# Optimization experiments

Measured on AMD Instinct MI355X. Metric: run time of the kernel, lower is better.

Reference implementation:

```python
import jax, jax.numpy as jnp
import numpy as np

LOG2PI = 1.8378770664093453
KL_WEIGHT = 1.0
N_OBS = 2_000_000
N_REFL = 250_000
N_IMG = 2000
MC = 32
N_OPS = 2
D_META = 6
D_EMB = 32
D_IN = 2 + 2 + D_META + 2 + D_EMB  # Imodel(2) + Iscale(2) + metadata(6) + wavelength + 1/d^2 + image embed
HIDDEN = 64


def weighted_pearson(x, y, w):
    z = 1.0 / w.sum(-1)
    mx = z * (w * x).sum(-1)
    my = z * (w * y).sum(-1)
    dx = x - mx
    dy = y - my
    cxy = z * (w * dx * dy).sum(-1)
    cx = z * (w * dx * dx).sum(-1)
    cy = z * (w * dy * dy).sum(-1)
    return cxy / jnp.sqrt(cx * cy)


def setup_inputs() -> dict:
    key = jax.random.key(0)
    ks = jax.random.split(key, 16)
    I = jax.random.normal(ks[0], (N_OBS, 1), jnp.float32)
    SigI = jax.random.uniform(ks[1], (N_OBS, 1), jnp.float32, 0.5, 1.5)
    image_id = jnp.sort(jax.random.randint(ks[2], (N_OBS,), 0, N_IMG, jnp.int32))
    metadata = jax.random.normal(ks[3], (N_OBS, D_META), jnp.float32)
    wavelength = 1.0 + 0.1 * jax.random.uniform(ks[4], (N_OBS, 1), jnp.float32)
    dHKL = jax.random.uniform(ks[5], (N_OBS, 1), jnp.float32, 1.0, 4.0)
    refl_ids = jax.random.randint(ks[6], (N_OPS, N_OBS), 0, N_REFL, jnp.int32)
    q_loc = jax.random.normal(ks[7], (N_REFL,), jnp.float32)
    q_scale_raw = 0.1 * jax.random.normal(ks[8], (N_REFL,), jnp.float32)
    img_emb = 0.1 * jax.random.normal(ks[9], (N_IMG, D_EMB), jnp.float32)
    W1 = jax.random.normal(ks[10], (D_IN, HIDDEN), jnp.float32) / np.sqrt(D_IN)
    b1 = jnp.zeros((HIDDEN,), jnp.float32)
    W2 = jax.random.normal(ks[11], (HIDDEN, 2), jnp.float32) / np.sqrt(HIDDEN)
    b2 = jnp.zeros((2,), jnp.float32)
    zeps = jax.random.normal(ks[12], (MC, N_REFL), jnp.float32)
    seps = jax.random.normal(ks[13], (N_OBS, MC), jnp.float32)
    return dict(I=I, SigI=SigI, image_id=image_id, metadata=metadata,
                wavelength=wavelength, dHKL=dHKL, refl_ids=refl_ids,
                q_loc=q_loc, q_scale_raw=q_scale_raw, img_emb=img_emb,
                W1=W1, b1=b1, W2=W2, b2=b2, zeps=zeps, seps=seps)


def reference(I, SigI, image_id, metadata, wavelength, dHKL, refl_ids,
              q_loc, q_scale_raw, img_emb, W1, b1, W2, b2, zeps, seps):
    n_images = img_emb.shape[0]
    sq = jax.nn.softplus(q_scale_raw)                         # q.stddev  [n_refl]
    # KL(N(q_loc, sq) || N(0, 1)), analytic, averaged over reflections
    kl_div = (-jnp.log(sq) + 0.5 * (sq * sq + q_loc * q_loc) - 0.5).mean()
    meta = jnp.concatenate([metadata, wavelength, 1.0 / jnp.square(dHKL)], -1)  # [N, 8]
    Iscale = jnp.concatenate([I, SigI], -1)                   # [N, 2]
    Imodel = jnp.stack([q_loc, sq], -1)                       # [n_refl, 2]
    zT = (q_loc[None, :] + sq[None, :] * zeps).T              # rsample, [n_refl, mc]
    emb = img_emb[image_id]                                   # [N, d_emb]
    ll_list, Ipred_list = [], []
    for op in range(refl_ids.shape[0]):                       # small fixed op count
        rid = refl_ids[op]                                    # [N]
        _Imodel = Imodel[rid]                                 # gather  [N, 2]
        feats = jnp.concatenate([_Imodel, Iscale, meta, emb], -1)
        h = jax.nn.relu(feats @ W1 + b1)
        loc_ls = h @ W2 + b2                                  # [N, 2]
        scale = loc_ls[:, :1] + jax.nn.softplus(loc_ls[:, 1:]) * seps  # [N, mc]
        _Ipred = zT[rid] * scale                              # gather * scale [N, mc]
        _ll = -0.5 * jnp.square((_Ipred - I) / SigI) - jnp.log(SigI) - 0.5 * LOG2PI
        _ll = jax.ops.segment_sum(_ll, image_id, num_segments=n_images)  # [n_img, mc]
        ll_list.append(_ll.mean(-1))                          # [n_img]
        Ipred_list.append(_Ipred.mean(-1))                    # [N]
    ll = jnp.stack(ll_list, -1)                               # [n_img, n_ops]
    ll_max = ll.max(-1)
    op_idx = ll.argmax(-1)                                    # [n_img]
    elbo = -ll_max.mean() + KL_WEIGHT * kl_div
    Ipred = jnp.stack(Ipred_list, -1)                         # [N, n_ops]
    sel = jnp.take_along_axis(Ipred, op_idx[image_id][:, None], -1)[:, 0]
    w = 1.0 / jnp.square(SigI)
    cc = weighted_pearson(I[:, 0], sel, w[:, 0])
    return jnp.stack([elbo, cc])
```

## Files before the change

kernel.cpp:

```cpp
#include <hip/hip_runtime.h>
#include <hip/hip_fp16.h>
#include <math.h>

#define N_OBS_C 2000000
#define N_REFL_C 250000
#define N_IMG_C 2000
#define MC_C 32
#define HID 64
#define NSLOT 16
#define LOG2PI_F 1.8378770664093453f


typedef float f2 __attribute__((ext_vector_type(2)));

__device__ __forceinline__ void pkfma(f2& d, f2 a, f2 b) {
    asm("v_pk_fma_f32 %0, %1, %2, %0" : "+v"(d) : "v"(a), "v"(b));
}
__device__ __forceinline__ f2 pkfma3(f2 a, f2 b, f2 c) {
    f2 d;
    asm("v_pk_fma_f32 %0, %1, %2, %3" : "=v"(d) : "v"(a), "v"(b), "v"(c));
    return d;
}

__device__ __forceinline__ float softplusf(float x) {
    return (x > 20.f) ? x : log1pf(expf(x));
}

#define ZERO_F4 96004
__global__ __launch_bounds__(256) void k_zero(float4* __restrict__ p) {
    int i = blockIdx.x * 256 + threadIdx.x;
    if (i < ZERO_F4) p[i] = make_float4(0.f, 0.f, 0.f, 0.f);
}

__global__ __launch_bounds__(256) void k_refl(const float* __restrict__ q_loc,
                                              const float* __restrict__ q_scale_raw,
                                              const float* __restrict__ zeps,
                                              float* __restrict__ sq,
                                              __half* __restrict__ zT,
                                              double* __restrict__ kl_sum) {
    int r = blockIdx.x * 256 + threadIdx.x;
    double kl = 0.0;
    if (r < N_REFL_C) {
        float ql = q_loc[r];
        float sp = softplusf(q_scale_raw[r]);
        sq[r] = sp;
        kl = (double)(-logf(sp) + 0.5f * (sp * sp + ql * ql) - 0.5f);
        float z[MC_C];
#pragma unroll
        for (int m = 0; m < MC_C; ++m)
            z[m] = fmaf(sp, zeps[(size_t)m * N_REFL_C + r], ql);
        uint4* outp = (uint4*)(zT + (size_t)r * MC_C);
#pragma unroll
        for (int q = 0; q < 4; ++q) {
            __half2 h0 = __floats2half2_rn(z[8 * q + 0], z[8 * q + 1]);
            __half2 h1 = __floats2half2_rn(z[8 * q + 2], z[8 * q + 3]);
            __half2 h2 = __floats2half2_rn(z[8 * q + 4], z[8 * q + 5]);
            __half2 h3 = __floats2half2_rn(z[8 * q + 6], z[8 * q + 7]);
            outp[q] = make_uint4(*(unsigned*)&h0, *(unsigned*)&h1,
                                 *(unsigned*)&h2, *(unsigned*)&h3);
        }
    }
    for (int o = 32; o > 0; o >>= 1) kl += __shfl_xor(kl, o);
    __shared__ double skl[4];
    int lane = threadIdx.x & 63, w = threadIdx.x >> 6;
    if (lane == 0) skl[w] = kl;
    __syncthreads();
    if (threadIdx.x == 0) atomicAdd(kl_sum, skl[0] + skl[1] + skl[2] + skl[3]);
}

__global__ __launch_bounds__(64) void k_imgpre(const float* __restrict__ img_emb,
                                               const float* __restrict__ W1,
                                               const float* __restrict__ b1,
                                               float* __restrict__ img_pre) {
    int g = blockIdx.x;
    int j = threadIdx.x;
    float acc = b1[j];
#pragma unroll
    for (int e = 0; e < 32; ++e)
        acc = fmaf(img_emb[g * 32 + e], W1[(12 + e) * HID + j], acc);
    img_pre[g * HID + j] = acc;
}

__global__ __launch_bounds__(256) void k_mlp(const float* __restrict__ I,
                                             const float* __restrict__ SigI,
                                             const int* __restrict__ image_id,
                                             const float* __restrict__ metadata,
                                             const float* __restrict__ wavelength,
                                             const float* __restrict__ dHKL,
                                             const int* __restrict__ refl_ids,
                                             const float* __restrict__ q_loc,
                                             const float* __restrict__ W1,
                                             const float* __restrict__ W2,
                                             const float* __restrict__ b2,
                                             const float* __restrict__ sq,
                                             const float* __restrict__ img_pre,
                                             float4* __restrict__ params) {
    __shared__ float sW1[12 * HID];
    __shared__ float sW2a[HID], sW2b[HID];
    for (int t = threadIdx.x; t < 12 * HID; t += 256) sW1[t] = W1[t];
    if (threadIdx.x < HID) {
        sW2a[threadIdx.x] = W2[threadIdx.x * 2 + 0];
        sW2b[threadIdx.x] = W2[threadIdx.x * 2 + 1];
    }
    __syncthreads();

    int n0 = blockIdx.x * 512 + threadIdx.x;
    int n1 = n0 + 256;
    bool a0 = (n0 < N_OBS_C), a1 = (n1 < N_OBS_C);
    int m0 = a0 ? n0 : (N_OBS_C - 1);
    int m1 = a1 ? n1 : (N_OBS_C - 1);

    f2 f0p[10], f1p[10];
    {
        float v;
        v = I[m0];            f0p[0].x = v; f0p[0].y = v;
        v = SigI[m0];         f0p[1].x = v; f0p[1].y = v;
#pragma unroll
        for (int i = 0; i < 6; ++i) {
            v = metadata[(size_t)m0 * 6 + i];
            f0p[2 + i].x = v; f0p[2 + i].y = v;
        }
        v = wavelength[m0];   f0p[8].x = v; f0p[8].y = v;
        float dh = dHKL[m0];
        v = 1.0f / (dh * dh); f0p[9].x = v; f0p[9].y = v;

        v = I[m1];            f1p[0].x = v; f1p[0].y = v;
        v = SigI[m1];         f1p[1].x = v; f1p[1].y = v;
#pragma unroll
        for (int i = 0; i < 6; ++i) {
            v = metadata[(size_t)m1 * 6 + i];
            f1p[2 + i].x = v; f1p[2 + i].y = v;
        }
        v = wavelength[m1];   f1p[8].x = v; f1p[8].y = v;
        dh = dHKL[m1];
        v = 1.0f / (dh * dh); f1p[9].x = v; f1p[9].y = v;
    }

    int g0 = image_id[m0], g1 = image_id[m1];
    int r00 = refl_ids[m0], r01 = refl_ids[N_OBS_C + m0];
    int r10 = refl_ids[m1], r11 = refl_ids[N_OBS_C + m1];
    f2 qa0p, sa0p, qb0p, sb0p, qa1p, sa1p, qb1p, sb1p;
    { float v;
      v = q_loc[r00]; qa0p.x = v; qa0p.y = v;
      v = sq[r00];    sa0p.x = v; sa0p.y = v;
      v = q_loc[r01]; qb0p.x = v; qb0p.y = v;
      v = sq[r01];    sb0p.x = v; sb0p.y = v;
      v = q_loc[r10]; qa1p.x = v; qa1p.y = v;
      v = sq[r10];    sa1p.x = v; sa1p.y = v;
      v = q_loc[r11]; qb1p.x = v; qb1p.y = v;
      v = sq[r11];    sb1p.x = v; sb1p.y = v;
    }
    const float* ip0 = img_pre + (size_t)g0 * HID;
    const float* ip1 = img_pre + (size_t)g1 * HID;

    f2 lA00 = {0.f, 0.f}, lA01 = {0.f, 0.f}, lB00 = {0.f, 0.f}, lB01 = {0.f, 0.f};
    f2 lA10 = {0.f, 0.f}, lA11 = {0.f, 0.f}, lB10 = {0.f, 0.f}, lB11 = {0.f, 0.f};

#pragma unroll 1
    for (int jt = 0; jt < HID; jt += 8) {
        f2 ac0[4], ac1[4];
        {
            float4 pa = *(const float4*)&ip0[jt];
            float4 pb = *(const float4*)&ip0[jt + 4];
            ac0[0].x = pa.x; ac0[0].y = pa.y;
            ac0[1].x = pa.z; ac0[1].y = pa.w;
            ac0[2].x = pb.x; ac0[2].y = pb.y;
            ac0[3].x = pb.z; ac0[3].y = pb.w;
            pa = *(const float4*)&ip1[jt];
            pb = *(const float4*)&ip1[jt + 4];
            ac1[0].x = pa.x; ac1[0].y = pa.y;
            ac1[1].x = pa.z; ac1[1].y = pa.w;
            ac1[2].x = pb.x; ac1[2].y = pb.y;
            ac1[3].x = pb.z; ac1[3].y = pb.w;
        }
#pragma unroll
        for (int i = 0; i < 10; ++i) {
            float4 wa = *(const float4*)&sW1[(i + 2) * HID + jt];
            float4 wb = *(const float4*)&sW1[(i + 2) * HID + jt + 4];
            f2 w0; w0.x = wa.x; w0.y = wa.y;
            f2 w1; w1.x = wa.z; w1.y = wa.w;
            f2 w2; w2.x = wb.x; w2.y = wb.y;
            f2 w3; w3.x = wb.z; w3.y = wb.w;
            pkfma(ac0[0], f0p[i], w0); pkfma(ac1[0], f1p[i], w0);
            pkfma(ac0[1], f0p[i], w1); pkfma(ac1[1], f1p[i], w1);
            pkfma(ac0[2], f0p[i], w2); pkfma(ac1[2], f1p[i], w2);
            pkfma(ac0[3], f0p[i], w3); pkfma(ac1[3], f1p[i], w3);
        }
        f2 w0p[4], w1p[4], vap[4], vbp[4];
        {
            float4 wa = *(const float4*)&sW1[jt];
            float4 wb = *(const float4*)&sW1[jt + 4];
            w0p[0].x = wa.x; w0p[0].y = wa.y;
            w0p[1].x = wa.z; w0p[1].y = wa.w;
            w0p[2].x = wb.x; w0p[2].y = wb.y;
            w0p[3].x = wb.z; w0p[3].y = wb.w;
            wa = *(const float4*)&sW1[HID + jt];
            wb = *(const float4*)&sW1[HID + jt + 4];
            w1p[0].x = wa.x; w1p[0].y = wa.y;
            w1p[1].x = wa.z; w1p[1].y = wa.w;
            w1p[2].x = wb.x; w1p[2].y = wb.y;
            w1p[3].x = wb.z; w1p[3].y = wb.w;
            wa = *(const float4*)&sW2a[jt];
            wb = *(const float4*)&sW2a[jt + 4];
            vap[0].x = wa.x; vap[0].y = wa.y;
            vap[1].x = wa.z; vap[1].y = wa.w;
            vap[2].x = wb.x; vap[2].y = wb.y;
            vap[3].x = wb.z; vap[3].y = wb.w;
            wa = *(const float4*)&sW2b[jt];
            wb = *(const float4*)&sW2b[jt + 4];
            vbp[0].x = wa.x; vbp[0].y = wa.y;
            vbp[1].x = wa.z; vbp[1].y = wa.w;
            vbp[2].x = wb.x; vbp[2].y = wb.y;
            vbp[3].x = wb.z; vbp[3].y = wb.w;
        }
#pragma unroll
        for (int k = 0; k < 4; ++k) {
            f2 h;
            h = pkfma3(sa0p, w1p[k], ac0[k]);
            pkfma(h, qa0p, w0p[k]);
            h.x = fmaxf(h.x, 0.f); h.y = fmaxf(h.y, 0.f);
            pkfma(lA00, h, vap[k]);
            pkfma(lA01, h, vbp[k]);
            h = pkfma3(sb0p, w1p[k], ac0[k]);
            pkfma(h, qb0p, w0p[k]);
            h.x = fmaxf(h.x, 0.f); h.y = fmaxf(h.y, 0.f);
            pkfma(lB00, h, vap[k]);
            pkfma(lB01, h, vbp[k]);
            h = pkfma3(sa1p, w1p[k], ac1[k]);
            pkfma(h, qa1p, w0p[k]);
            h.x = fmaxf(h.x, 0.f); h.y = fmaxf(h.y, 0.f);
            pkfma(lA10, h, vap[k]);
            pkfma(lA11, h, vbp[k]);
            h = pkfma3(sb1p, w1p[k], ac1[k]);
            pkfma(h, qb1p, w0p[k]);
            h.x = fmaxf(h.x, 0.f); h.y = fmaxf(h.y, 0.f);
            pkfma(lB10, h, vap[k]);
            pkfma(lB11, h, vbp[k]);
        }
    }

    float bb0 = b2[0], bb1 = b2[1];
    if (a0) {
        float la0 = bb0 + lA00.x + lA00.y;
        float la1 = bb1 + lA01.x + lA01.y;
        float lb0 = bb0 + lB00.x + lB00.y;
        float lb1 = bb1 + lB01.x + lB01.y;
        params[n0] = make_float4(la0, softplusf(la1), lb0, softplusf(lb1));
    }
    if (a1) {
        float la0 = bb0 + lA10.x + lA10.y;
        float la1 = bb1 + lA11.x + lA11.y;
        float lb0 = bb0 + lB10.x + lB10.y;
        float lb1 = bb1 + lB11.x + lB11.y;
        params[n1] = make_float4(la0, softplusf(la1), lb0, softplusf(lb1));
    }
}

__global__ __launch_bounds__(256) void k_mc(const float* __restrict__ I,
                                            const float* __restrict__ SigI,
                                            const int* __restrict__ image_id,
                                            const int* __restrict__ refl_ids,
                                            const float4* __restrict__ params,
                                            const float* __restrict__ seps,
                                            const __half* __restrict__ zT,
                                            float* __restrict__ img_mom) {
    int t = threadIdx.x;
    int base = blockIdx.x * 32;

    __shared__ float4 sPP[32];
    __shared__ float sIv[32], sSv[32];
    __shared__ int sG[32], sR0[32], sR1[32];
    {
        int f = t >> 5, o = t & 31;
        if (f == 0)      sPP[o] = params[base + o];
        else if (f == 1) sIv[o] = I[base + o];
        else if (f == 2) sSv[o] = SigI[base + o];
        else if (f == 3) sG[o]  = image_id[base + o];
        else if (f == 4) sR0[o] = refl_ids[base + o];
        else if (f == 5) sR1[o] = refl_ids[N_OBS_C + base + o];
    }
    __syncthreads();

    int grp = t >> 3;
    int m4 = t & 7;
    int n = base + grp;

    float In = sIv[grp];
    float Sn = sSv[grp];
    int rid0 = sR0[grp];
    int rid1 = sR1[grp];
    float4 pp = sPP[grp];

    float4 ss = *(const float4*)&seps[(size_t)n * MC_C + m4 * 4];
    float4 z0, z1;
    {
        const __half2* zp = (const __half2*)(zT + (size_t)rid0 * MC_C + m4 * 4);
        __half2 h0 = zp[0], h1 = zp[1];
        float2 fa = __half22float2(h0), fb = __half22float2(h1);
        z0 = make_float4(fa.x, fa.y, fb.x, fb.y);
        zp = (const __half2*)(zT + (size_t)rid1 * MC_C + m4 * 4);
        h0 = zp[0]; h1 = zp[1];
        fa = __half22float2(h0); fb = __half22float2(h1);
        z1 = make_float4(fa.x, fa.y, fb.x, fb.y);
    }

    float rsig = 1.0f / Sn;
    float mnIr = -In * rsig;

    float sd20 = 0.f, sip0 = 0.f, sd21 = 0.f, sip1 = 0.f;
#define MCSTEP(zc0, zc1, sc_)                              \
    {                                                      \
        float sc0 = fmaf(pp.y, sc_, pp.x);                 \
        float ip0 = zc0 * sc0;                             \
        float d0 = fmaf(ip0, rsig, mnIr);                  \
        sd20 = fmaf(d0, d0, sd20);                         \
        sip0 += ip0;                                       \
        float sc1 = fmaf(pp.w, sc_, pp.z);                 \
        float ip1 = zc1 * sc1;                             \
        float d1 = fmaf(ip1, rsig, mnIr);                  \
        sd21 = fmaf(d1, d1, sd21);                         \
        sip1 += ip1;                                       \
    }
    MCSTEP(z0.x, z1.x, ss.x)
    MCSTEP(z0.y, z1.y, ss.y)
    MCSTEP(z0.z, z1.z, ss.z)
    MCSTEP(z0.w, z1.w, ss.w)
#undef MCSTEP

#pragma unroll
    for (int o = 4; o > 0; o >>= 1) {
        sd20 += __shfl_xor(sd20, o);
        sd21 += __shfl_xor(sd21, o);
        sip0 += __shfl_xor(sip0, o);
        sip1 += __shfl_xor(sip1, o);
    }

    __shared__ float mom[32][12];
    __shared__ int sameflag;
    if (m4 == 0) {
        float logS32 = 32.f * logf(Sn) + 16.f * LOG2PI_F;
        float y0 = sip0 * (1.0f / 32.0f);
        float y1 = sip1 * (1.0f / 32.0f);
        float w = rsig * rsig;
        mom[grp][0] = -0.5f * sd20 - logS32;
        mom[grp][1] = -0.5f * sd21 - logS32;
        mom[grp][2] = w;
        mom[grp][3] = w * In;
        mom[grp][4] = w * In * In;
        mom[grp][5] = w * y0;
        mom[grp][6] = w * y0 * y0;
        mom[grp][7] = w * In * y0;
        mom[grp][8] = w * y1;
        mom[grp][9] = w * y1 * y1;
        mom[grp][10] = w * In * y1;
        mom[grp][11] = 0.f;
    }
    __syncthreads();
    if (t == 0) {
        bool same = true;
        int g0 = sG[0];
#pragma unroll
        for (int s = 1; s < 32; ++s) same = same && (sG[s] == g0);
        sameflag = same;
    }
    __syncthreads();
    int slot = blockIdx.x & (NSLOT - 1);
    if (t < 12) {
        if (sameflag) {
            float a = 0.f;
#pragma unroll
            for (int s = 0; s < 32; ++s) a += mom[s][t];
            atomicAdd(&img_mom[(sG[0] * 12 + t) * NSLOT + slot], a);
        } else {
            for (int s = 0; s < 32; ++s)
                atomicAdd(&img_mom[(sG[s] * 12 + t) * NSLOT + slot], mom[s][t]);
        }
    }
}

__global__ __launch_bounds__(256) void k_img(const float* __restrict__ img_mom,
                                             double* __restrict__ accs) {
    int g = blockIdx.x * 256 + threadIdx.x;
    double red7[7] = {0, 0, 0, 0, 0, 0, 0};
    if (g < N_IMG_C) {
        float M[12];
#pragma unroll
        for (int j = 0; j < 12; ++j) {
            const float4* p = (const float4*)&img_mom[(g * 12 + j) * NSLOT];
            float4 q0 = p[0], q1 = p[1], q2 = p[2], q3 = p[3];
            M[j] = (q0.x + q0.y + q0.z + q0.w) + (q1.x + q1.y + q1.z + q1.w) +
                   (q2.x + q2.y + q2.z + q2.w) + (q3.x + q3.y + q3.z + q3.w);
        }
        float ll0 = M[0] * (1.0f / 32.0f);
        float ll1 = M[1] * (1.0f / 32.0f);
        bool op1 = (ll1 > ll0);
        red7[0] = (double)fmaxf(ll0, ll1);
        red7[1] = (double)M[2];
        red7[2] = (double)M[3];
        red7[3] = (double)(op1 ? M[8] : M[5]);
        red7[4] = (double)M[4];
        red7[5] = (double)(op1 ? M[9] : M[6]);
        red7[6] = (double)(op1 ? M[10] : M[7]);
    }
#pragma unroll
    for (int k = 0; k < 7; ++k)
        for (int o = 32; o > 0; o >>= 1) red7[k] += __shfl_xor(red7[k], o);
    __shared__ double sred[4][7];
    int lane = threadIdx.x & 63, w = threadIdx.x >> 6;
    if (lane == 0) {
#pragma unroll
        for (int k = 0; k < 7; ++k) sred[w][k] = red7[k];
    }
    __syncthreads();
    if (threadIdx.x < 7) {
        double v = sred[0][threadIdx.x] + sred[1][threadIdx.x] +
                   sred[2][threadIdx.x] + sred[3][threadIdx.x];
        atomicAdd(&accs[1 + threadIdx.x], v);
    }
}

__global__ void k_final(const double* __restrict__ accs, float* __restrict__ out) {
    double kl = accs[0] / (double)N_REFL_C;
    double elbo = -(accs[1] / (double)N_IMG_C) + 1.0 * kl;
    double W = accs[2], Sx = accs[3], Sy = accs[4];
    double Sxx = accs[5], Syy = accs[6], Sxy = accs[7];
    double z = 1.0 / W;
    double mx = z * Sx, my = z * Sy;
    double cxy = z * Sxy - mx * my;
    double cx = z * Sxx - mx * mx;
    double cy = z * Syy - my * my;
    double cc = cxy / sqrt(cx * cy);
    out[0] = (float)elbo;
    out[1] = (float)cc;
}

extern "C" void kernel_launch(void* const* d_in, const int* in_sizes, int n_in,
                              void* d_out, int out_size, void* d_ws, size_t ws_size,
                              hipStream_t stream) {
    const float* I = (const float*)d_in[0];
    const float* SigI = (const float*)d_in[1];
    const int* image_id = (const int*)d_in[2];
    const float* metadata = (const float*)d_in[3];
    const float* wavelength = (const float*)d_in[4];
    const float* dHKL = (const float*)d_in[5];
    const int* refl_ids = (const int*)d_in[6];
    const float* q_loc = (const float*)d_in[7];
    const float* q_scale_raw = (const float*)d_in[8];
    const float* img_emb = (const float*)d_in[9];
    const float* W1 = (const float*)d_in[10];
    const float* b1 = (const float*)d_in[11];
    const float* W2 = (const float*)d_in[12];
    const float* b2 = (const float*)d_in[13];
    const float* zeps = (const float*)d_in[14];
    const float* seps = (const float*)d_in[15];
    float* out = (float*)d_out;

    char* ws = (char*)d_ws;
    double* accs = (double*)ws;
    float* img_mom = (float*)(ws + 64);
    float* sqv = (float*)(ws + 2097152);
    float* img_pre = (float*)(ws + 4194304);
    __half* zT = (__half*)(ws + 8388608);
    float4* params = (float4*)(ws + 50331648);

    k_zero<<<(ZERO_F4 + 255) / 256, 256, 0, stream>>>((float4*)ws);
    k_refl<<<(N_REFL_C + 255) / 256, 256, 0, stream>>>(q_loc, q_scale_raw, zeps,
                                                       sqv, zT, &accs[0]);
    k_imgpre<<<N_IMG_C, 64, 0, stream>>>(img_emb, W1, b1, img_pre);
    k_mlp<<<(N_OBS_C + 511) / 512, 256, 0, stream>>>(I, SigI, image_id, metadata,
                                                     wavelength, dHKL, refl_ids,
                                                     q_loc, W1, W2, b2, sqv,
                                                     img_pre, params);
    k_mc<<<N_OBS_C / 32, 256, 0, stream>>>(I, SigI, image_id, refl_ids,
                                           params, seps, zT, img_mom);
    k_img<<<(N_IMG_C + 255) / 256, 256, 0, stream>>>(img_mom, accs);
    k_final<<<1, 1, 0, stream>>>(accs, out);
}
```

Baseline: 264.6 us.

## Process 64 observations per block in MC kernel with wider loads and ballot reduction

New measurement: 352.3 us. +33.2%, slower.

```diff
diff --git a/kernel.cpp b/kernel.cpp
--- a/kernel.cpp
+++ b/kernel.cpp
@@ -265,24 +265,24 @@
                                             const __half* __restrict__ zT,
                                             float* __restrict__ img_mom) {
     int t = threadIdx.x;
-    int base = blockIdx.x * 32;
-
-    __shared__ float4 sPP[32];
-    __shared__ float sIv[32], sSv[32];
-    __shared__ int sG[32], sR0[32], sR1[32];
-    {
-        int f = t >> 5, o = t & 31;
+    int base = blockIdx.x * 64;
+
+    __shared__ float4 sPP[64];
+    __shared__ float sIv[64], sSv[64];
+    __shared__ int sG[64], sR0[64], sR1[64];
+    for (int idx = t; idx < 384; idx += 256) {
+        int f = idx >> 6, o = idx & 63;
         if (f == 0)      sPP[o] = params[base + o];
         else if (f == 1) sIv[o] = I[base + o];
         else if (f == 2) sSv[o] = SigI[base + o];
         else if (f == 3) sG[o]  = image_id[base + o];
         else if (f == 4) sR0[o] = refl_ids[base + o];
-        else if (f == 5) sR1[o] = refl_ids[N_OBS_C + base + o];
+        else             sR1[o] = refl_ids[N_OBS_C + base + o];
     }
     __syncthreads();
 
-    int grp = t >> 3;
-    int m4 = t & 7;
+    int grp = t >> 2;
+    int m8 = t & 3;
     int n = base + grp;
 
     float In = sIv[grp];
@@ -291,17 +291,27 @@
     int rid1 = sR1[grp];
     float4 pp = sPP[grp];
 
-    float4 ss = *(const float4*)&seps[(size_t)n * MC_C + m4 * 4];
-    float4 z0, z1;
+    const float4* sp4 = (const float4*)&seps[(size_t)n * MC_C + m8 * 8];
+    float4 ssA = sp4[0], ssB = sp4[1];
+
+    float4 z0A, z0B, z1A, z1B;
     {
-        const __half2* zp = (const __half2*)(zT + (size_t)rid0 * MC_C + m4 * 4);
-        __half2 h0 = zp[0], h1 = zp[1];
-        float2 fa = __half22float2(h0), fb = __half22float2(h1);
-        z0 = make_float4(fa.x, fa.y, fb.x, fb.y);
-        zp = (const __half2*)(zT + (size_t)rid1 * MC_C + m4 * 4);
-        h0 = zp[0]; h1 = zp[1];
-        fa = __half22float2(h0); fb = __half22float2(h1);
-        z1 = make_float4(fa.x, fa.y, fb.x, fb.y);
+        uint4 u = *(const uint4*)(zT + (size_t)rid0 * MC_C + m8 * 8);
+        __half2 h;
+        float2 fa, fb;
+        *(unsigned*)&h = u.x; fa = __half22float2(h);
+        *(unsigned*)&h = u.y; fb = __half22float2(h);
+        z0A = make_float4(fa.x, fa.y, fb.x, fb.y);
+        *(unsigned*)&h = u.z; fa = __half22float2(h);
+        *(unsigned*)&h = u.w; fb = __half22float2(h);
+        z0B = make_float4(fa.x, fa.y, fb.x, fb.y);
+        u = *(const uint4*)(zT + (size_t)rid1 * MC_C + m8 * 8);
+        *(unsigned*)&h = u.x; fa = __half22float2(h);
+        *(unsigned*)&h = u.y; fb = __half22float2(h);
+        z1A = make_float4(fa.x, fa.y, fb.x, fb.y);
+        *(unsigned*)&h = u.z; fa = __half22float2(h);
+        *(unsigned*)&h = u.w; fb = __half22float2(h);
+        z1B = make_float4(fa.x, fa.y, fb.x, fb.y);
     }
 
     float rsig = 1.0f / Sn;
@@ -321,23 +331,26 @@
         sd21 = fmaf(d1, d1, sd21);                         \
         sip1 += ip1;                                       \
     }
-    MCSTEP(z0.x, z1.x, ss.x)
-    MCSTEP(z0.y, z1.y, ss.y)
-    MCSTEP(z0.z, z1.z, ss.z)
-    MCSTEP(z0.w, z1.w, ss.w)
+    MCSTEP(z0A.x, z1A.x, ssA.x)
+    MCSTEP(z0A.y, z1A.y, ssA.y)
+    MCSTEP(z0A.z, z1A.z, ssA.z)
+    MCSTEP(z0A.w, z1A.w, ssA.w)
+    MCSTEP(z0B.x, z1B.x, ssB.x)
+    MCSTEP(z0B.y, z1B.y, ssB.y)
+    MCSTEP(z0B.z, z1B.z, ssB.z)
+    MCSTEP(z0B.w, z1B.w, ssB.w)
 #undef MCSTEP
 
 #pragma unroll
-    for (int o = 4; o > 0; o >>= 1) {
+    for (int o = 2; o > 0; o >>= 1) {
         sd20 += __shfl_xor(sd20, o);
         sd21 += __shfl_xor(sd21, o);
         sip0 += __shfl_xor(sip0, o);
         sip1 += __shfl_xor(sip1, o);
     }
 
-    __shared__ float mom[32][12];
-    __shared__ int sameflag;
-    if (m4 == 0) {
+    __shared__ float mom[64][13];
+    if (m8 == 0) {
         float logS32 = 32.f * logf(Sn) + 16.f * LOG2PI_F;
         float y0 = sip0 * (1.0f / 32.0f);
         float y1 = sip1 * (1.0f / 32.0f);
@@ -356,24 +369,25 @@
         mom[grp][11] = 0.f;
     }
     __syncthreads();
-    if (t == 0) {
-        bool same = true;
+    if (t < 64) {
+        int s = t;
         int g0 = sG[0];
-#pragma unroll
-        for (int s = 1; s < 32; ++s) same = same && (sG[s] == g0);
-        sameflag = same;
-    }
-    __syncthreads();
-    int slot = blockIdx.x & (NSLOT - 1);
-    if (t < 12) {
-        if (sameflag) {
-            float a = 0.f;
-#pragma unroll
-            for (int s = 0; s < 32; ++s) a += mom[s][t];
-            atomicAdd(&img_mom[(sG[0] * 12 + t) * NSLOT + slot], a);
+        int gs = sG[s];
+        unsigned long long bal = __ballot(gs == g0);
+        bool allsame = (bal == 0xFFFFFFFFFFFFFFFFull);
+        int slot = blockIdx.x & (NSLOT - 1);
+        if (allsame) {
+#pragma unroll
+            for (int j = 0; j < 12; ++j) {
+                float v = mom[s][j];
+#pragma unroll
+                for (int o = 32; o > 0; o >>= 1) v += __shfl_xor(v, o);
+                if (s == 0) atomicAdd(&img_mom[(g0 * 12 + j) * NSLOT + slot], v);
+            }
         } else {
-            for (int s = 0; s < 32; ++s)
-                atomicAdd(&img_mom[(sG[s] * 12 + t) * NSLOT + slot], mom[s][t]);
+#pragma unroll
+            for (int j = 0; j < 12; ++j)
+                atomicAdd(&img_mom[(gs * 12 + j) * NSLOT + slot], mom[s][j]);
         }
     }
 }
@@ -471,7 +485,7 @@
                                                      wavelength, dHKL, refl_ids,
                                                      q_loc, W1, W2, b2, sqv,
                                                      img_pre, params);
-    k_mc<<<N_OBS_C / 32, 256, 0, stream>>>(I, SigI, image_id, refl_ids,
+    k_mc<<<N_OBS_C / 64, 256, 0, stream>>>(I, SigI, image_id, refl_ids,
                                            params, seps, zT, img_mom);
     k_img<<<(N_IMG_C + 255) / 256, 256, 0, stream>>>(img_mom, accs);
     k_final<<<1, 1, 0, stream>>>(accs, out);
```
